# Kernel tuning notes

Hardware: AMD Instinct MI355X
Metric: run time of the kernel (lower is better)

## Reference

```python
import jax, jax.numpy as jnp
import numpy as np

B, S, DIM = 4, 1024, 2048
HQ, HKV, HD = 16, 4, 128  # query heads, kv heads, head dim
G = HQ // HKV             # GQA group size


def _rope(t, freqs):
    # t: (B, S, H, HD); freqs: (S, HD//2) angles. Llama-style: adjacent pairs
    # (even, odd) treated as (real, imag) and rotated by exp(i*theta).
    tr = t.reshape(t.shape[:-1] + (HD // 2, 2))
    cos = jnp.cos(freqs)[None, :, None, :]
    sin = jnp.sin(freqs)[None, :, None, :]
    re = tr[..., 0] * cos - tr[..., 1] * sin
    im = tr[..., 0] * sin + tr[..., 1] * cos
    return jnp.stack([re, im], axis=-1).reshape(t.shape)


def setup_inputs() -> dict:
    key = jax.random.key(0)
    ks = jax.random.split(key, 5)
    x = jax.random.normal(ks[0], (B, S, DIM), jnp.float32)
    # rotary angles: outer(t, 1/10000^(2i/d))
    inv_freq = 1.0 / (10000.0 ** (np.arange(0, HD, 2, dtype=np.float32) / HD))
    freqs = jnp.asarray(np.outer(np.arange(S, dtype=np.float32), inv_freq))
    # additive causal mask (finite large negative for numerical safety)
    i = jnp.arange(S)
    mask = jnp.where(i[None, :] <= i[:, None], 0.0, -1e9).astype(jnp.float32)
    std = 0.02
    wq = jax.random.normal(ks[1], (HQ * HD, DIM), jnp.float32) * std
    wk = jax.random.normal(ks[2], (HKV * HD, DIM), jnp.float32) * std
    wv = jax.random.normal(ks[3], (HKV * HD, DIM), jnp.float32) * std
    wo = jax.random.normal(ks[4], (DIM, DIM), jnp.float32) * std
    return {"x": x, "start_pos": 0, "freqs": freqs, "mask": mask,
            "wq": wq, "wk": wk, "wv": wv, "wo": wo}


def reference(x, start_pos, freqs, mask, wq, wk, wv, wo):
    b, s, _ = x.shape
    q = (x @ wq.T).reshape(b, s, HQ, HD)
    k = (x @ wk.T).reshape(b, s, HKV, HD)
    v = (x @ wv.T).reshape(b, s, HKV, HD)
    q = _rope(q, freqs)
    k = _rope(k, freqs)
    # GQA: group query heads per kv head, avoiding repeat_kv materialization
    qg = q.reshape(b, s, HKV, G, HD)
    scores = jnp.einsum('bskgd,btkd->bkgst', qg, k) / np.float32(np.sqrt(HD))
    scores = scores + mask  # (S,S) broadcasts over (b, kv, g, s, t)
    p = jax.nn.softmax(scores, axis=-1)
    o = jnp.einsum('bkgst,btkd->bskgd', p, v).reshape(b, s, HQ * HD)
    return o @ wo.T
```

## Files before the change

### kernel.cpp

```cpp
#include <hip/hip_runtime.h>

typedef unsigned short u16;
typedef unsigned int u32;
typedef __bf16 bf16x8 __attribute__((ext_vector_type(8)));
typedef float floatx4 __attribute__((ext_vector_type(4)));

__device__ __forceinline__ u16 f2bf(float x) {
  union { float f; u32 u; } v; v.f = x;
  u32 r = v.u + 0x7fffu + ((v.u >> 16) & 1u);
  return (u16)(r >> 16);
}
__device__ __forceinline__ float bf2f(u16 x) {
  union { float f; u32 u; } v; v.u = ((u32)x) << 16;
  return v.f;
}

__device__ __forceinline__ void gl_lds16(const u16* g, u16* l) {
  __builtin_amdgcn_global_load_lds((const __attribute__((address_space(1))) void*)g,
                                   (__attribute__((address_space(3))) void*)l, 16, 0, 0);
}

__global__ __launch_bounds__(256) void cvt_all(const float* __restrict__ x,
                                               const float* __restrict__ wq,
                                               const float* __restrict__ wk,
                                               const float* __restrict__ wv,
                                               const float* __restrict__ wo,
                                               u16* __restrict__ xb, u16* __restrict__ wqb,
                                               u16* __restrict__ wkb, u16* __restrict__ wvb,
                                               u16* __restrict__ wob) {
  int i = blockIdx.x * 256 + threadIdx.x;
  const float* s; u16* d; int off;
  if (i < 2097152)      { s = x;  d = xb;  off = 0; }
  else if (i < 3145728) { s = wq; d = wqb; off = 2097152; }
  else if (i < 3407872) { s = wk; d = wkb; off = 3145728; }
  else if (i < 3670016) { s = wv; d = wvb; off = 3407872; }
  else                  { s = wo; d = wob; off = 3670016; }
  i -= off;
  float4 v = ((const float4*)s)[i];
  uint2 o;
  o.x = (u32)f2bf(v.x) | ((u32)f2bf(v.y) << 16);
  o.y = (u32)f2bf(v.z) | ((u32)f2bf(v.w) << 16);
  ((uint2*)d)[i] = o;
}

__global__ __launch_bounds__(256) void rope_both(u16* __restrict__ qb, u16* __restrict__ kb,
                                                 const float* __restrict__ fr) {
  int idx = blockIdx.x * 256 + threadIdx.x;
  u16* t; int lgH; float scale;
  if (idx < 4194304) { t = qb; lgH = 4; scale = 0.08838834764831845f; }
  else               { t = kb; lgH = 2; scale = 1.0f; idx -= 4194304; }
  int p = idx & 63;
  int bsh = idx >> 6;
  int s = (bsh >> lgH) & 1023;
  float th = fr[s * 64 + p];
  float sn, cs;
  sincosf(th, &sn, &cs);
  u32* base = (u32*)(t + (size_t)bsh * 128 + p * 2);
  u32 pr = *base;
  float e = bf2f((u16)(pr & 0xffffu));
  float o = bf2f((u16)(pr >> 16));
  u16 re = f2bf((e * cs - o * sn) * scale);
  u16 im = f2bf((e * sn + o * cs) * scale);
  *base = (u32)re | ((u32)im << 16);
}

__device__ __forceinline__ void gemm_core(const u16* __restrict__ A, const u16* __restrict__ Bw,
                                          u16* sA, u16* sB, int m0, int n0,
                                          floatx4 acc[4][4]) {
  const int tid = threadIdx.x;
  const int wave = tid >> 6, lane = tid & 63;
  const int quad = lane >> 4, l16 = lane & 15;
  const int wm = (wave >> 1) * 64, wn = (wave & 1) * 64;
  const int srow = wave * 8 + (lane >> 3);
  const int scol = (((lane & 7) ^ ((lane >> 3) & 7)) * 8);
  const int lds_off = wave * 512 + lane * 8;
  const int swA = (l16 & 7);
  for (int k0 = 0; k0 < 2048; k0 += 64) {
    __syncthreads();
    #pragma unroll
    for (int c = 0; c < 4; c++) {
      gl_lds16(A + (size_t)(m0 + c * 32 + srow) * 2048 + k0 + scol, sA + c * 2048 + lds_off);
      gl_lds16(Bw + (size_t)(n0 + c * 32 + srow) * 2048 + k0 + scol, sB + c * 2048 + lds_off);
    }
    __syncthreads();
    #pragma unroll
    for (int ks = 0; ks < 64; ks += 32) {
      const int pc = ((((ks >> 3) + quad) ^ swA) << 3);
      bf16x8 af[4], bw[4];
      #pragma unroll
      for (int i = 0; i < 4; i++)
        af[i] = *(const bf16x8*)&sA[(wm + i * 16 + l16) * 64 + pc];
      #pragma unroll
      for (int j = 0; j < 4; j++)
        bw[j] = *(const bf16x8*)&sB[(wn + j * 16 + l16) * 64 + pc];
      #pragma unroll
      for (int i = 0; i < 4; i++)
        #pragma unroll
        for (int j = 0; j < 4; j++)
          acc[i][j] = __builtin_amdgcn_mfma_f32_16x16x32_bf16(af[i], bw[j], acc[i][j], 0, 0, 0);
    }
  }
}

__global__ __launch_bounds__(256, 2) void gemm_qkv(const u16* __restrict__ xb,
                                                   const u16* __restrict__ wqb,
                                                   const u16* __restrict__ wkb,
                                                   const u16* __restrict__ wvb,
                                                   u16* __restrict__ qb, u16* __restrict__ kb,
                                                   u16* __restrict__ vtb) {
  __shared__ __align__(16) u16 sA[128 * 64];
  __shared__ __align__(16) u16 sB[128 * 64];
  const int by = blockIdx.y;
  const u16* Bw; int n0, mode;
  if (by < 16)      { Bw = wqb; n0 = by * 128;        mode = 0; }
  else if (by < 20) { Bw = wkb; n0 = (by - 16) * 128; mode = 1; }
  else              { Bw = wvb; n0 = (by - 20) * 128; mode = 2; }
  const int m0 = blockIdx.x * 128;
  floatx4 acc[4][4] = {};
  gemm_core(xb, Bw, sA, sB, m0, n0, acc);
  const int tid = threadIdx.x;
  const int wave = tid >> 6, lane = tid & 63;
  const int quad = lane >> 4, l16 = lane & 15;
  const int wm = (wave >> 1) * 64, wn = (wave & 1) * 64;
  #pragma unroll
  for (int i = 0; i < 4; i++) {
    #pragma unroll
    for (int j = 0; j < 4; j++) {
      const int row0 = m0 + wm + i * 16 + quad * 4;
      const int col = n0 + wn + j * 16 + l16;
      #pragma unroll
      for (int r = 0; r < 4; r++) {
        int m = row0 + r;
        u16 val = f2bf(acc[i][j][r]);
        if (mode == 0) {
          qb[(size_t)m * 2048 + col] = val;
        } else if (mode == 1) {
          kb[(size_t)m * 512 + col] = val;
        } else {
          int b = m >> 10, sI = m & 1023, kvh = col >> 7, hd = col & 127;
          vtb[((size_t)((b * 4 + kvh) * 128 + hd)) * 1024 + sI] = val;
        }
      }
    }
  }
}

__global__ __launch_bounds__(256, 2) void gemm_out(const u16* __restrict__ ob,
                                                   const u16* __restrict__ wob,
                                                   float* __restrict__ Cf) {
  __shared__ __align__(16) u16 sA[128 * 64];
  __shared__ __align__(16) u16 sB[128 * 64];
  const int m0 = blockIdx.x * 128, n0 = blockIdx.y * 128;
  floatx4 acc[4][4] = {};
  gemm_core(ob, wob, sA, sB, m0, n0, acc);
  const int tid = threadIdx.x;
  const int wave = tid >> 6, lane = tid & 63;
  const int quad = lane >> 4, l16 = lane & 15;
  const int wm = (wave >> 1) * 64, wn = (wave & 1) * 64;
  #pragma unroll
  for (int i = 0; i < 4; i++) {
    #pragma unroll
    for (int j = 0; j < 4; j++) {
      const int row0 = m0 + wm + i * 16 + quad * 4;
      const int col = n0 + wn + j * 16 + l16;
      #pragma unroll
      for (int r = 0; r < 4; r++)
        Cf[(size_t)(row0 + r) * 2048 + col] = acc[i][j][r];
    }
  }
}

__device__ __forceinline__ void attn_chunk(const u16* __restrict__ qbaseHead,
                                           const u16* __restrict__ kbase,
                                           const u16* __restrict__ vbase,
                                           int qr0, int kt_begin, int kt_end,
                                           u16* myP, floatx4 (&o_acc)[2][8],
                                           float (&l_part)[2], int quad, int l16) {
  const floatx4 vzero = {0.f, 0.f, 0.f, 0.f};
  #pragma unroll
  for (int i = 0; i < 2; i++) {
    l_part[i] = 0.f;
    #pragma unroll
    for (int j = 0; j < 8; j++) o_acc[i][j] = vzero;
  }
  bf16x8 aq[2][4];
  #pragma unroll
  for (int i = 0; i < 2; i++)
    #pragma unroll
    for (int ks = 0; ks < 4; ks++)
      aq[i][ks] = *(const bf16x8*)(qbaseHead + (size_t)(qr0 + i * 16 + l16) * 2048 + ks * 32 + quad * 8);

  bf16x8 bk[2][4];
  #pragma unroll
  for (int j = 0; j < 4; j++)
    bk[0][j] = *(const bf16x8*)(kbase + (size_t)(kt_begin * 64 + j * 16 + l16) * 512 + quad * 8);

  for (int kt = kt_begin; kt < kt_end; kt++) {
    const int t0 = kt * 64;
    const int t0n = (kt + 1 < kt_end) ? t0 + 64 : t0;
    floatx4 s_acc[4][2];
    #pragma unroll
    for (int j = 0; j < 4; j++)
      #pragma unroll
      for (int i = 0; i < 2; i++) s_acc[j][i] = vzero;
    bf16x8 bv[2][8];
    #pragma unroll
    for (int j2 = 0; j2 < 8; j2++)
      bv[0][j2] = *(const bf16x8*)(vbase + (size_t)(j2 * 16 + l16) * 1024 + t0 + quad * 8);
    #pragma unroll
    for (int ks = 0; ks < 4; ks++) {
      const int nks = (ks + 1) & 3;
      const int nt0 = (ks == 3) ? t0n : t0;
      #pragma unroll
      for (int j = 0; j < 4; j++)
        bk[(ks + 1) & 1][j] =
            *(const bf16x8*)(kbase + (size_t)(nt0 + j * 16 + l16) * 512 + nks * 32 + quad * 8);
      #pragma unroll
      for (int j = 0; j < 4; j++)
        #pragma unroll
        for (int i = 0; i < 2; i++)
          s_acc[j][i] = __builtin_amdgcn_mfma_f32_16x16x32_bf16(bk[ks & 1][j], aq[i][ks], s_acc[j][i], 0, 0, 0);
    }
    #pragma unroll
    for (int j2 = 0; j2 < 8; j2++)
      bv[1][j2] = *(const bf16x8*)(vbase + (size_t)(j2 * 16 + l16) * 1024 + t0 + 32 + quad * 8);
    #pragma unroll
    for (int i = 0; i < 2; i++) {
      const int qrow = qr0 + i * 16 + l16;
      #pragma unroll
      for (int j = 0; j < 4; j++) {
        const int key0 = t0 + j * 16 + quad * 4;
        float e0 = (key0 + 0 <= qrow) ? __expf(s_acc[j][i][0]) : 0.f;
        float e1 = (key0 + 1 <= qrow) ? __expf(s_acc[j][i][1]) : 0.f;
        float e2 = (key0 + 2 <= qrow) ? __expf(s_acc[j][i][2]) : 0.f;
        float e3 = (key0 + 3 <= qrow) ? __expf(s_acc[j][i][3]) : 0.f;
        l_part[i] += (e0 + e1) + (e2 + e3);
        uint2 w;
        w.x = (u32)f2bf(e0) | ((u32)f2bf(e1) << 16);
        w.y = (u32)f2bf(e2) | ((u32)f2bf(e3) << 16);
        *(uint2*)&myP[(i * 16 + l16) * 68 + j * 16 + quad * 4] = w;
      }
    }
    #pragma unroll
    for (int ks2 = 0; ks2 < 2; ks2++) {
      bf16x8 ap[2];
      #pragma unroll
      for (int i = 0; i < 2; i++)
        ap[i] = *(const bf16x8*)&myP[(i * 16 + l16) * 68 + ks2 * 32 + quad * 8];
      #pragma unroll
      for (int i = 0; i < 2; i++)
        #pragma unroll
        for (int j2 = 0; j2 < 8; j2++)
          o_acc[i][j2] = __builtin_amdgcn_mfma_f32_16x16x32_bf16(ap[i], bv[ks2][j2], o_acc[i][j2], 0, 0, 0);
    }
  }
}

__device__ __forceinline__ void store_out(u16* __restrict__ obaseHead, int qr0,
                                          floatx4 (&o_acc)[2][8], float (&l_part)[2],
                                          int quad, int l16) {
  #pragma unroll
  for (int i = 0; i < 2; i++) {
    float lr = l_part[i];
    lr += __shfl_xor(lr, 16);
    lr += __shfl_xor(lr, 32);
    #pragma unroll
    for (int r = 0; r < 4; r++) {
      const float inv = 1.f / __shfl(lr, quad * 4 + r);
      const int row = qr0 + i * 16 + quad * 4 + r;
      #pragma unroll
      for (int j = 0; j < 8; j++)
        obaseHead[(size_t)row * 2048 + j * 16 + l16] = f2bf(o_acc[i][j][r] * inv);
    }
  }
}

__global__ __launch_bounds__(256)
__attribute__((amdgpu_waves_per_eu(2, 2)))
void flash_attn(const u16* __restrict__ q,
                const u16* __restrict__ k,
                const u16* __restrict__ vt,
                u16* __restrict__ o) {
  __shared__ __align__(16) char smem[52224];
  const int tid = threadIdx.x;
  const int wave = tid >> 6, lane = tid & 63;
  const int quad = lane >> 4, l16 = lane & 15;
  const int pr = wave >> 1, role = wave & 1;
  const int bi = blockIdx.x;
  const int h = bi & 63;
  const int b = h >> 4, hq = h & 15, kv = (hq >> 2);
  const int pair = (bi >> 6) * 2 + pr;
  const int p = pair, qc = 31 - pair;
  const int Tp = (32 * p + 31) / 64 + 1, Tq = (32 * qc + 31) / 64 + 1;
  const int tA = (Tp + Tq) >> 1;
  u16* myP = (u16*)(smem + wave * 4352);
  float* ldsO = (float*)(smem + 17408 + pr * 17408);
  float* ldsL = (float*)(smem + 17408 + pr * 17408 + 16896);

  const u16* qbaseHead = q + (size_t)b * 2097152 + hq * 128;
  const u16* kbase = k + (size_t)b * 524288 + kv * 128;
  const u16* vbase = vt + (size_t)(b * 4 + kv) * 131072;
  u16* obaseHead = o + (size_t)b * 2097152 + hq * 128;

  floatx4 o_acc[2][8];
  float l_part[2];
  if (role == 0) {
    attn_chunk(qbaseHead, kbase, vbase, qc * 32, 0, tA, myP, o_acc, l_part, quad, l16);
    #pragma unroll
    for (int i = 0; i < 2; i++) {
      ldsL[i * 64 + lane] = l_part[i];
      #pragma unroll
      for (int j = 0; j < 8; j++)
        #pragma unroll
        for (int r = 0; r < 4; r++)
          ldsO[(i * 16 + quad * 4 + r) * 132 + j * 16 + l16] = o_acc[i][j][r];
    }
    __syncthreads();
  } else {
    attn_chunk(qbaseHead, kbase, vbase, p * 32, 0, Tp, myP, o_acc, l_part, quad, l16);
    store_out(obaseHead, p * 32, o_acc, l_part, quad, l16);
    attn_chunk(qbaseHead, kbase, vbase, qc * 32, tA, Tq, myP, o_acc, l_part, quad, l16);
    __syncthreads();
    #pragma unroll
    for (int i = 0; i < 2; i++) {
      l_part[i] += ldsL[i * 64 + lane];
      #pragma unroll
      for (int j = 0; j < 8; j++)
        #pragma unroll
        for (int r = 0; r < 4; r++)
          o_acc[i][j][r] += ldsO[(i * 16 + quad * 4 + r) * 132 + j * 16 + l16];
    }
    store_out(obaseHead, qc * 32, o_acc, l_part, quad, l16);
  }
}

extern "C" void kernel_launch(void* const* d_in, const int* in_sizes, int n_in,
                              void* d_out, int out_size, void* d_ws, size_t ws_size,
                              hipStream_t stream) {
  const float* x  = (const float*)d_in[0];
  const float* fr = (const float*)d_in[2];
  const float* wq = (const float*)d_in[4];
  const float* wk = (const float*)d_in[5];
  const float* wv = (const float*)d_in[6];
  const float* wo = (const float*)d_in[7];
  float* out = (float*)d_out;

  char* ws = (char*)d_ws;
  u16* xb  = (u16*)(ws + 0);
  u16* wqb = (u16*)(ws + 16777216);
  u16* wkb = (u16*)(ws + 25165824);
  u16* wvb = (u16*)(ws + 27262976);
  u16* wob = (u16*)(ws + 29360128);
  u16* qb  = (u16*)(ws + 37748736);
  u16* kb  = (u16*)(ws + 54525952);
  u16* vtb = (u16*)(ws + 58720256);
  u16* ob  = (u16*)(ws + 62914560);

  cvt_all<<<18432, 256, 0, stream>>>(x, wq, wk, wv, wo, xb, wqb, wkb, wvb, wob);
  gemm_qkv<<<dim3(32, 24), 256, 0, stream>>>(xb, wqb, wkb, wvb, qb, kb, vtb);
  rope_both<<<20480, 256, 0, stream>>>(qb, kb, fr);
  flash_attn<<<512, 256, 0, stream>>>(qb, kb, vtb, ob);
  gemm_out<<<dim3(32, 16), 256, 0, stream>>>(ob, wob, out);
}
```

Baseline: 316.3 us.

## Split attention into per-chunk 2-wave blocks, use exp2 with folded log2e, skip masking

New measurement: 400.7 us. 1.27x slower.

```diff
diff --git a/kernel.cpp b/kernel.cpp
--- a/kernel.cpp
+++ b/kernel.cpp
@@ -4,6 +4,12 @@
 typedef unsigned int u32;
 typedef __bf16 bf16x8 __attribute__((ext_vector_type(8)));
 typedef float floatx4 __attribute__((ext_vector_type(4)));
+
+#if __has_builtin(__builtin_amdgcn_exp2f)
+#define EXP2F(x) __builtin_amdgcn_exp2f(x)
+#else
+#define EXP2F(x) __expf((x) * 0.6931471805599453f)
+#endif
 
 __device__ __forceinline__ u16 f2bf(float x) {
   union { float f; u32 u; } v; v.f = x;
@@ -47,7 +53,7 @@
                                                  const float* __restrict__ fr) {
   int idx = blockIdx.x * 256 + threadIdx.x;
   u16* t; int lgH; float scale;
-  if (idx < 4194304) { t = qb; lgH = 4; scale = 0.08838834764831845f; }
+  if (idx < 4194304) { t = qb; lgH = 4; scale = 0.08838834764831845f * 1.4426950408889634f; }
   else               { t = kb; lgH = 2; scale = 1.0f; idx -= 4194304; }
   int p = idx & 63;
   int bsh = idx >> 6;
@@ -102,7 +108,7 @@
   }
 }
 
-__global__ __launch_bounds__(256, 2) void gemm_qkv(const u16* __restrict__ xb,
+__global__ __launch_bounds__(256, 3) void gemm_qkv(const u16* __restrict__ xb,
                                                    const u16* __restrict__ wqb,
                                                    const u16* __restrict__ wkb,
                                                    const u16* __restrict__ wvb,
@@ -145,7 +151,7 @@
   }
 }
 
-__global__ __launch_bounds__(256, 2) void gemm_out(const u16* __restrict__ ob,
+__global__ __launch_bounds__(256, 3) void gemm_out(const u16* __restrict__ ob,
                                                    const u16* __restrict__ wob,
                                                    float* __restrict__ Cf) {
   __shared__ __align__(16) u16 sA[128 * 64];
@@ -224,16 +230,25 @@
     #pragma unroll
     for (int j2 = 0; j2 < 8; j2++)
       bv[1][j2] = *(const bf16x8*)(vbase + (size_t)(j2 * 16 + l16) * 1024 + t0 + 32 + quad * 8);
+    const bool nomask = (t0 + 63 <= qr0);
     #pragma unroll
     for (int i = 0; i < 2; i++) {
       const int qrow = qr0 + i * 16 + l16;
       #pragma unroll
       for (int j = 0; j < 4; j++) {
         const int key0 = t0 + j * 16 + quad * 4;
-        float e0 = (key0 + 0 <= qrow) ? __expf(s_acc[j][i][0]) : 0.f;
-        float e1 = (key0 + 1 <= qrow) ? __expf(s_acc[j][i][1]) : 0.f;
-        float e2 = (key0 + 2 <= qrow) ? __expf(s_acc[j][i][2]) : 0.f;
-        float e3 = (key0 + 3 <= qrow) ? __expf(s_acc[j][i][3]) : 0.f;
+        float e0, e1, e2, e3;
+        if (nomask) {
+          e0 = EXP2F(s_acc[j][i][0]);
+          e1 = EXP2F(s_acc[j][i][1]);
+          e2 = EXP2F(s_acc[j][i][2]);
+          e3 = EXP2F(s_acc[j][i][3]);
+        } else {
+          e0 = (key0 + 0 <= qrow) ? EXP2F(s_acc[j][i][0]) : 0.f;
+          e1 = (key0 + 1 <= qrow) ? EXP2F(s_acc[j][i][1]) : 0.f;
+          e2 = (key0 + 2 <= qrow) ? EXP2F(s_acc[j][i][2]) : 0.f;
+          e3 = (key0 + 3 <= qrow) ? EXP2F(s_acc[j][i][3]) : 0.f;
+        }
         l_part[i] += (e0 + e1) + (e2 + e3);
         uint2 w;
         w.x = (u32)f2bf(e0) | ((u32)f2bf(e1) << 16);
@@ -275,27 +290,24 @@
   }
 }
 
-__global__ __launch_bounds__(256)
-__attribute__((amdgpu_waves_per_eu(2, 2)))
+__global__ __launch_bounds__(128, 3)
 void flash_attn(const u16* __restrict__ q,
                 const u16* __restrict__ k,
                 const u16* __restrict__ vt,
                 u16* __restrict__ o) {
-  __shared__ __align__(16) char smem[52224];
+  __shared__ __align__(16) char smem[26112];
   const int tid = threadIdx.x;
   const int wave = tid >> 6, lane = tid & 63;
   const int quad = lane >> 4, l16 = lane & 15;
-  const int pr = wave >> 1, role = wave & 1;
   const int bi = blockIdx.x;
   const int h = bi & 63;
   const int b = h >> 4, hq = h & 15, kv = (hq >> 2);
-  const int pair = (bi >> 6) * 2 + pr;
-  const int p = pair, qc = 31 - pair;
-  const int Tp = (32 * p + 31) / 64 + 1, Tq = (32 * qc + 31) / 64 + 1;
-  const int tA = (Tp + Tq) >> 1;
+  const int c = 31 - (bi >> 6);
+  const int Tc = (32 * c + 31) / 64 + 1;
+  const int tMid = Tc >> 1;
   u16* myP = (u16*)(smem + wave * 4352);
-  float* ldsO = (float*)(smem + 17408 + pr * 17408);
-  float* ldsL = (float*)(smem + 17408 + pr * 17408 + 16896);
+  float* ldsO = (float*)(smem + 8704);
+  float* ldsL = (float*)(smem + 8704 + 16896);
 
   const u16* qbaseHead = q + (size_t)b * 2097152 + hq * 128;
   const u16* kbase = k + (size_t)b * 524288 + kv * 128;
@@ -304,8 +316,8 @@
 
   floatx4 o_acc[2][8];
   float l_part[2];
-  if (role == 0) {
-    attn_chunk(qbaseHead, kbase, vbase, qc * 32, 0, tA, myP, o_acc, l_part, quad, l16);
+  if (wave == 0) {
+    attn_chunk(qbaseHead, kbase, vbase, c * 32, 0, tMid, myP, o_acc, l_part, quad, l16);
     #pragma unroll
     for (int i = 0; i < 2; i++) {
       ldsL[i * 64 + lane] = l_part[i];
@@ -317,9 +329,7 @@
     }
     __syncthreads();
   } else {
-    attn_chunk(qbaseHead, kbase, vbase, p * 32, 0, Tp, myP, o_acc, l_part, quad, l16);
-    store_out(obaseHead, p * 32, o_acc, l_part, quad, l16);
-    attn_chunk(qbaseHead, kbase, vbase, qc * 32, tA, Tq, myP, o_acc, l_part, quad, l16);
+    attn_chunk(qbaseHead, kbase, vbase, c * 32, tMid, Tc, myP, o_acc, l_part, quad, l16);
     __syncthreads();
     #pragma unroll
     for (int i = 0; i < 2; i++) {
@@ -330,7 +340,7 @@
         for (int r = 0; r < 4; r++)
           o_acc[i][j][r] += ldsO[(i * 16 + quad * 4 + r) * 132 + j * 16 + l16];
     }
-    store_out(obaseHead, qc * 32, o_acc, l_part, quad, l16);
+    store_out(obaseHead, c * 32, o_acc, l_part, quad, l16);
   }
 }
 
@@ -359,6 +369,6 @@
   cvt_all<<<18432, 256, 0, stream>>>(x, wq, wk, wv, wo, xb, wqb, wkb, wvb, wob);
   gemm_qkv<<<dim3(32, 24), 256, 0, stream>>>(xb, wqb, wkb, wvb, qb, kb, vtb);
   rope_both<<<20480, 256, 0, stream>>>(qb, kb, fr);
-  flash_attn<<<512, 256, 0, stream>>>(qb, kb, vtb, ob);
+  flash_attn<<<2048, 128, 0, stream>>>(qb, kb, vtb, ob);
   gemm_out<<<dim3(32, 16), 256, 0, stream>>>(ob, wob, out);
 }
```
